# Kernel tuning notes

Measured on AMD Instinct MI355X. Metric: run time of the kernel, lower is better.

The kernel has to match this reference:

```python
import jax, jax.numpy as jnp
import numpy as np

B, D, F, FH = 8, 16, 16, 128
L = D * D
EPS = 1e-5


def _coords():
    i = np.arange(L, dtype=np.float64)
    c0 = ((i + 1) / D - D / 2) / (D / 2)
    c1 = ((i + 1) % D - D / 2) / (D / 2)
    return jnp.asarray(np.stack([c0, c1], axis=1), dtype=jnp.float32)  # (L, 2)


def setup_inputs() -> dict:
    key = jax.random.key(0)
    ks = jax.random.split(key, 16)
    s = 0.05
    fin = F + 2
    inp = {
        "x": jax.random.normal(ks[0], (B, F, D, D), jnp.float32),
        # g_fc1 weight split into the x_i half (first f+2 cols) and x_j half
        "W1a": jax.random.normal(ks[1], (fin, FH), jnp.float32) * s,
        "W1b": jax.random.normal(ks[2], (fin, FH), jnp.float32) * s,
        "b1": jnp.zeros((FH,), jnp.float32),
        "g1_gamma": jnp.ones((FH,), jnp.float32), "g1_beta": jnp.zeros((FH,), jnp.float32),
        "W2": jax.random.normal(ks[3], (FH, FH), jnp.float32) * s, "b2": jnp.zeros((FH,), jnp.float32),
        "g2_gamma": jnp.ones((FH,), jnp.float32), "g2_beta": jnp.zeros((FH,), jnp.float32),
        "W3": jax.random.normal(ks[4], (FH, FH), jnp.float32) * s, "b3": jnp.zeros((FH,), jnp.float32),
        "g3_gamma": jnp.ones((FH,), jnp.float32), "g3_beta": jnp.zeros((FH,), jnp.float32),
        "Wagg": jax.random.normal(ks[5], (L,), jnp.float32) * s, "bagg": jnp.zeros((), jnp.float32),
        "Wf": jax.random.normal(ks[6], (FH, FH), jnp.float32) * s, "bf": jnp.zeros((FH,), jnp.float32),
        "f_gamma": jnp.ones((FH,), jnp.float32), "f_beta": jnp.zeros((FH,), jnp.float32),
        "Wo2": jax.random.normal(ks[7], (FH, FH), jnp.float32) * s, "bo2": jnp.zeros((FH,), jnp.float32),
        "o2_gamma": jnp.ones((FH,), jnp.float32), "o2_beta": jnp.zeros((FH,), jnp.float32),
        "Wo3": jax.random.normal(ks[8], (FH, F), jnp.float32) * s, "bo3": jnp.zeros((F,), jnp.float32),
        "coord": _coords(),
    }
    return inp


def _bn(h, gamma, beta):
    # torch BatchNorm1d (training mode) applied over channel dim = last axis here;
    # stats over (batch, length), biased variance.
    mu = jnp.mean(h, axis=(0, 1))
    var = jnp.mean((h - mu) ** 2, axis=(0, 1))
    return gamma * (h - mu) * jax.lax.rsqrt(var + EPS) + beta


def reference(x, W1a, W1b, b1, g1_gamma, g1_beta, W2, b2, g2_gamma, g2_beta,
              W3, b3, g3_gamma, g3_beta, Wagg, bagg, Wf, bf, f_gamma, f_beta,
              Wo2, bo2, o2_gamma, o2_beta, Wo3, bo3, coord):
    b, f, d = x.shape[0], x.shape[1], x.shape[2]
    l = d * d
    x_flat = x.reshape(b, f, l).transpose(0, 2, 1)                     # (b, L, f)
    x_flat = jnp.concatenate([x_flat, jnp.broadcast_to(coord, (b, l, 2))], axis=2)  # (b, L, f+2)
    # g_fc1 on cat([x_i, x_j]): x_i varies along pair-dim2 (index l), x_j along dim1 (index k)
    hi = x_flat @ W1a                                                  # (b, L, FH)
    hj = x_flat @ W1b                                                  # (b, L, FH)
    h = hi[:, None, :, :] + hj[:, :, None, :] + b1                     # (b, L, L, FH)
    h = h.reshape(b, l * l, -1)
    h = jax.nn.relu(_bn(h, g1_gamma, g1_beta))
    h = jax.nn.relu(_bn(h @ W2 + b2, g2_gamma, g2_beta))
    h = jax.nn.relu(_bn(h @ W3 + b3, g3_gamma, g3_beta))
    x_g = h.reshape(b, l, l, -1)                                       # (b, k, l, FH)
    # affine_aggregate: Linear(L -> 1) over the l (dim2) axis after permute
    x_agg = jnp.einsum('bklf,l->bkf', x_g, Wagg) + bagg                # (b, L, FH)
    x_f = jax.nn.relu(_bn(x_agg @ Wf + bf, f_gamma, f_beta))
    xo = jax.nn.relu(_bn(x_f @ Wo2 + bo2, o2_gamma, o2_beta))
    out = xo @ Wo3 + bo3                                               # (b, L, f)
    return out.reshape(b, d, d, f).transpose(0, 3, 1, 2)               # (b, f, d, d)
```

## Files before the change

kernel.cpp:

```cpp
#include <hip/hip_runtime.h>
#include <hip/hip_bf16.h>

typedef __bf16 bf16x8 __attribute__((ext_vector_type(8)));
typedef float  f32x4  __attribute__((ext_vector_type(4)));

static constexpr size_t MB = 1u << 20;
static constexpr size_t HI_OFF  = 0;
static constexpr size_t HJ_OFF  = HI_OFF + MB;
static constexpr size_t Z_OFF   = HJ_OFF + MB;
static constexpr size_t PS_OFF  = Z_OFF + (size_t)524288 * 128 * 2;
static constexpr size_t PQ_OFF  = PS_OFF + (size_t)4096 * 128 * 4;
static constexpr size_t S1I_OFF = PQ_OFF + (size_t)4096 * 128 * 4;
static constexpr size_t S2I_OFF = S1I_OFF + 32768;
static constexpr size_t S1J_OFF = S2I_OFF + 32768;
static constexpr size_t S2J_OFF = S1J_OFF + 32768;
static constexpr size_t A1_OFF  = S2J_OFF + 32768;
static constexpr size_t D1_OFF  = A1_OFF + 512;
static constexpr size_t A2_OFF  = D1_OFF + 512;
static constexpr size_t C2_OFF  = A2_OFF + 512;
static constexpr size_t A3_OFF  = C2_OFF + 512;
static constexpr size_t C3_OFF  = A3_OFF + 512;
static constexpr size_t AF_OFF  = C3_OFF + 512;
static constexpr size_t CF_OFF  = AF_OFF + 512;
static constexpr size_t AO_OFF  = CF_OFF + 512;
static constexpr size_t CO_OFF  = AO_OFF + 512;
static constexpr size_t W2T_OFF = CO_OFF + 512;
static constexpr size_t W3T_OFF = W2T_OFF + 32768;
static constexpr size_t XAGG_OFF = W3T_OFF + 32768;
static constexpr size_t Y1_OFF  = XAGG_OFF + MB;
static constexpr size_t Y2_OFF  = Y1_OFF + MB;
static constexpr size_t TPS_OFF = Y2_OFF + MB;
static constexpr size_t TPQ_OFF = TPS_OFF + 65536;

__global__ void build_h(const float* __restrict__ x, const float* __restrict__ coord,
                        const float* __restrict__ W1a, const float* __restrict__ W1b,
                        float* __restrict__ hi, float* __restrict__ hj)
{
    __shared__ float xr[18];
    int bl = blockIdx.x;
    int b = bl >> 8, l = bl & 255;
    int t = threadIdx.x;
    if (t < 18)
        xr[t] = (t < 16) ? x[((size_t)b * 16 + t) * 256 + l] : coord[l * 2 + (t - 16)];
    __syncthreads();
    float ai = 0.f, aj = 0.f;
#pragma unroll
    for (int c = 0; c < 18; ++c) {
        float xv = xr[c];
        ai += xv * W1a[c * 128 + t];
        aj += xv * W1b[c * 128 + t];
    }
    hi[(size_t)bl * 128 + t] = ai;
    hj[(size_t)bl * 128 + t] = aj;
}

__global__ void stats1(const float* __restrict__ hi, const float* __restrict__ hj,
                       float* __restrict__ S1i, float* __restrict__ S2i,
                       float* __restrict__ S1j, float* __restrict__ S2j)
{
    int g = blockIdx.x;
    int b = g >> 3, lg = g & 7;
    int f = threadIdx.x;
    float s1i = 0, s2i = 0, s1j = 0, s2j = 0;
#pragma unroll 4
    for (int i = 0; i < 32; ++i) {
        int l = lg * 32 + i;
        float vi = hi[((size_t)b * 256 + l) * 128 + f];
        float vj = hj[((size_t)b * 256 + l) * 128 + f];
        s1i += vi; s2i += vi * vi;
        s1j += vj; s2j += vj * vj;
    }
    S1i[g * 128 + f] = s1i; S2i[g * 128 + f] = s2i;
    S1j[g * 128 + f] = s1j; S2j[g * 128 + f] = s2j;
}

__global__ void bn1_finalize(const float* __restrict__ S1i, const float* __restrict__ S2i,
                             const float* __restrict__ S1j, const float* __restrict__ S2j,
                             const float* __restrict__ g, const float* __restrict__ be,
                             float* __restrict__ a1, float* __restrict__ d1)
{
    int f = threadIdx.x;
    float s1i = 0, s2i = 0, s1j = 0, s2j = 0;
    float mib[8], mjb[8];
#pragma unroll
    for (int b = 0; b < 8; ++b) {
        float sb = 0, sbj = 0;
#pragma unroll
        for (int lg = 0; lg < 8; ++lg) {
            int gg = b * 8 + lg;
            sb  += S1i[gg * 128 + f]; s2i += S2i[gg * 128 + f];
            sbj += S1j[gg * 128 + f]; s2j += S2j[gg * 128 + f];
        }
        mib[b] = sb * (1.f / 256.f); mjb[b] = sbj * (1.f / 256.f);
        s1i += sb; s1j += sbj;
    }
    const float invN = 1.f / 2048.f;
    float mi = s1i * invN, mj = s1j * invN;
    float vu = s2i * invN - mi * mi;
    float vv = s2j * invN - mj * mj;
    float cr = 0.f;
#pragma unroll
    for (int b = 0; b < 8; ++b) cr += (mib[b] - mi) * (mjb[b] - mj);
    cr *= (1.f / 8.f);
    float var = vu + vv + 2.f * cr;
    float av = g[f] * rsqrtf(var + 1e-5f);
    a1[f] = av;
    d1[f] = be[f] - av * (mi + mj);
}

__global__ void transpose_w(const float* __restrict__ W2, const float* __restrict__ W3,
                            __bf16* __restrict__ W2t, __bf16* __restrict__ W3t)
{
    int f = blockIdx.x, k = threadIdx.x;
    W2t[f * 128 + k] = (__bf16)W2[k * 128 + f];
    W3t[f * 128 + k] = (__bf16)W3[k * 128 + f];
}

__global__ __launch_bounds__(256, 4) void pair_gemm1(
    const float* __restrict__ hi, const float* __restrict__ hj,
    const float* __restrict__ a1, const float* __restrict__ d1,
    const __bf16* __restrict__ W2t,
    __bf16* __restrict__ Z, float* __restrict__ ps, float* __restrict__ pq)
{
    __shared__ __align__(16) char hA[32768];

    int blk = blockIdx.x;
    int half = blk & 1;
    int bk = blk >> 1;
    int b = bk >> 8;
    int t = threadIdx.x;
    int lane = t & 63;
    int wave = t >> 6;
    int fc = (t & 15) * 8;
    int rg = t >> 4;
    int cl = lane & 15;
    int kg = lane >> 4;
    int colbase = wave * 32;

    bf16x8 Bf[2][4];
#pragma unroll
    for (int n = 0; n < 2; ++n) {
        const __bf16* wp = W2t + (colbase + n * 16 + cl) * 128 + kg * 8;
#pragma unroll
        for (int kk = 0; kk < 4; ++kk)
            Bf[n][kk] = *reinterpret_cast<const bf16x8*>(wp + kk * 32);
    }

    float a1v[8], qv[8];
    const float* hjrow = hj + (size_t)bk * 128 + fc;
    const float* d1p = d1 + fc;
    const float* a1p = a1 + fc;
#pragma unroll
    for (int j = 0; j < 8; ++j) { a1v[j] = a1p[j]; qv[j] = a1v[j] * hjrow[j] + d1p[j]; }

    const float* hib = hi + ((size_t)b * 256 + half * 128) * 128;
#pragma unroll
    for (int rr = 0; rr < 128; rr += 16) {
        int row = rr + rg;
        const float* src = hib + row * 128 + fc;
        bf16x8 v;
#pragma unroll
        for (int j = 0; j < 8; ++j) {
            float h = fmaxf(a1v[j] * src[j] + qv[j], 0.f);
            v[j] = (__bf16)h;
        }
        int byte = (row * 256 + fc * 2) ^ ((row & 7) << 4);
        *reinterpret_cast<bf16x8*>(hA + byte) = v;
    }
    __syncthreads();

    f32x4 acc[8][2] = {};
#pragma unroll
    for (int kk = 0; kk < 128; kk += 32) {
        bf16x8 af[8];
#pragma unroll
        for (int m = 0; m < 8; ++m) {
            int row = m * 16 + cl;
            int byte = (row * 256 + (kk + kg * 8) * 2) ^ ((row & 7) << 4);
            af[m] = *reinterpret_cast<const bf16x8*>(hA + byte);
        }
#pragma unroll
        for (int m = 0; m < 8; ++m)
#pragma unroll
            for (int n = 0; n < 2; ++n)
                acc[m][n] = __builtin_amdgcn_mfma_f32_16x16x32_bf16(af[m], Bf[n][kk >> 5], acc[m][n], 0, 0, 0);
    }

    __bf16* zb = Z + ((size_t)bk * 256 + half * 128) * 128;
    int r0 = kg * 4;
    float s[2] = {}, q[2] = {};
#pragma unroll
    for (int m = 0; m < 8; ++m)
#pragma unroll
        for (int r = 0; r < 4; ++r) {
            int row = m * 16 + r0 + r;
#pragma unroll
            for (int n = 0; n < 2; ++n) {
                float v = acc[m][n][r];
                zb[row * 128 + colbase + n * 16 + cl] = (__bf16)v;
                s[n] += v; q[n] += v * v;
            }
        }
#pragma unroll
    for (int n = 0; n < 2; ++n) {
        float sv = s[n], qv2 = q[n];
        sv += __shfl_xor(sv, 16); sv += __shfl_xor(sv, 32);
        qv2 += __shfl_xor(qv2, 16); qv2 += __shfl_xor(qv2, 32);
        if (lane < 16) {
            ps[(size_t)blk * 128 + colbase + n * 16 + cl] = sv;
            pq[(size_t)blk * 128 + colbase + n * 16 + cl] = qv2;
        }
    }
}

__global__ __launch_bounds__(256, 4) void pair_gemm2(
    __bf16* __restrict__ Z,
    const float* __restrict__ a2, const float* __restrict__ c2,
    const __bf16* __restrict__ W3t,
    float* __restrict__ ps, float* __restrict__ pq)
{
    __shared__ __align__(16) char hA[32768];

    int blk = blockIdx.x;
    int half = blk & 1;
    int bk = blk >> 1;
    int t = threadIdx.x;
    int lane = t & 63;
    int wave = t >> 6;
    int fc = (t & 15) * 8;
    int rg = t >> 4;
    int cl = lane & 15;
    int kg = lane >> 4;
    int colbase = wave * 32;

    bf16x8 Bf[2][4];
#pragma unroll
    for (int n = 0; n < 2; ++n) {
        const __bf16* wp = W3t + (colbase + n * 16 + cl) * 128 + kg * 8;
#pragma unroll
        for (int kk = 0; kk < 4; ++kk)
            Bf[n][kk] = *reinterpret_cast<const bf16x8*>(wp + kk * 32);
    }

    float a2v[8], c2v[8];
#pragma unroll
    for (int j = 0; j < 8; ++j) { a2v[j] = a2[fc + j]; c2v[j] = c2[fc + j]; }

    __bf16* zbase = Z + ((size_t)bk * 256 + half * 128) * 128;
#pragma unroll
    for (int rr = 0; rr < 128; rr += 16) {
        int row = rr + rg;
        bf16x8 zv = *reinterpret_cast<const bf16x8*>(zbase + row * 128 + fc);
        bf16x8 v;
#pragma unroll
        for (int j = 0; j < 8; ++j) {
            float h = fmaxf(a2v[j] * (float)zv[j] + c2v[j], 0.f);
            v[j] = (__bf16)h;
        }
        int byte = (row * 256 + fc * 2) ^ ((row & 7) << 4);
        *reinterpret_cast<bf16x8*>(hA + byte) = v;
    }
    __syncthreads();

    f32x4 acc[8][2] = {};
#pragma unroll
    for (int kk = 0; kk < 128; kk += 32) {
        bf16x8 af[8];
#pragma unroll
        for (int m = 0; m < 8; ++m) {
            int row = m * 16 + cl;
            int byte = (row * 256 + (kk + kg * 8) * 2) ^ ((row & 7) << 4);
            af[m] = *reinterpret_cast<const bf16x8*>(hA + byte);
        }
#pragma unroll
        for (int m = 0; m < 8; ++m)
#pragma unroll
            for (int n = 0; n < 2; ++n)
                acc[m][n] = __builtin_amdgcn_mfma_f32_16x16x32_bf16(af[m], Bf[n][kk >> 5], acc[m][n], 0, 0, 0);
    }

    int r0 = kg * 4;
    float s[2] = {}, q[2] = {};
#pragma unroll
    for (int m = 0; m < 8; ++m)
#pragma unroll
        for (int r = 0; r < 4; ++r) {
            int row = m * 16 + r0 + r;
#pragma unroll
            for (int n = 0; n < 2; ++n) {
                float v = acc[m][n][r];
                zbase[row * 128 + colbase + n * 16 + cl] = (__bf16)v;
                s[n] += v; q[n] += v * v;
            }
        }
#pragma unroll
    for (int n = 0; n < 2; ++n) {
        float sv = s[n], qv2 = q[n];
        sv += __shfl_xor(sv, 16); sv += __shfl_xor(sv, 32);
        qv2 += __shfl_xor(qv2, 16); qv2 += __shfl_xor(qv2, 32);
        if (lane < 16) {
            ps[(size_t)blk * 128 + colbase + n * 16 + cl] = sv;
            pq[(size_t)blk * 128 + colbase + n * 16 + cl] = qv2;
        }
    }
}

__global__ void finalize_bn(const float* __restrict__ ps, const float* __restrict__ pq,
                            int nblk, float inv_count,
                            const float* __restrict__ gamma, const float* __restrict__ beta,
                            float* __restrict__ a, float* __restrict__ c)
{
    __shared__ float rs[256], rq[256];
    int f = blockIdx.x, t = threadIdx.x;
    float s = 0, q = 0;
    for (int i = t; i < nblk; i += 256) {
        s += ps[(size_t)i * 128 + f];
        q += pq[(size_t)i * 128 + f];
    }
    rs[t] = s; rq[t] = q;
    __syncthreads();
    for (int st = 128; st > 0; st >>= 1) {
        if (t < st) { rs[t] += rs[t + st]; rq[t] += rq[t + st]; }
        __syncthreads();
    }
    if (t == 0) {
        float mean = rs[0] * inv_count;
        float var = rq[0] * inv_count - mean * mean;
        float av = gamma[f] * rsqrtf(var + 1e-5f);
        a[f] = av;
        c[f] = beta[f] - av * mean;
    }
}

__global__ __launch_bounds__(256) void aggregate(
    const __bf16* __restrict__ Z,
    const float* __restrict__ a3, const float* __restrict__ c3,
    const float* __restrict__ Wagg, const float* __restrict__ bagg,
    float* __restrict__ xagg)
{
    __shared__ float red[16 * 128];
    int bk = blockIdx.x;
    int t = threadIdx.x;
    int fc = t & 15;
    int g = t >> 4;
    float av[8], cv[8];
#pragma unroll
    for (int j = 0; j < 8; ++j) { av[j] = a3[fc * 8 + j]; cv[j] = c3[fc * 8 + j]; }

    const __bf16* zb = Z + (size_t)bk * 256 * 128;
    float acc[8] = {};
#pragma unroll 4
    for (int i = 0; i < 16; ++i) {
        int l = g * 16 + i;
        bf16x8 zv = *reinterpret_cast<const bf16x8*>(zb + (size_t)l * 128 + fc * 8);
        float w = Wagg[l];
#pragma unroll
        for (int j = 0; j < 8; ++j)
            acc[j] += fmaxf(av[j] * (float)zv[j] + cv[j], 0.f) * w;
    }
#pragma unroll
    for (int j = 0; j < 8; ++j) red[g * 128 + fc * 8 + j] = acc[j];
    __syncthreads();
    if (t < 128) {
        float s = 0;
#pragma unroll
        for (int gg = 0; gg < 16; ++gg) s += red[gg * 128 + t];
        xagg[(size_t)bk * 128 + t] = s + bagg[0];
    }
}

__global__ void tail_gemm(const float* __restrict__ X,
                          const float* __restrict__ aIn, const float* __restrict__ cIn, int relu_in,
                          const float* __restrict__ W, const float* __restrict__ bias,
                          float* __restrict__ Y, float* __restrict__ ps, float* __restrict__ pq)
{
    __shared__ float xs[2048];
    __shared__ float rsum[256];
    int blk = blockIdx.x, t = threadIdx.x;
    for (int i = t; i < 2048; i += 256) {
        float v = X[(size_t)blk * 2048 + i];
        if (relu_in) { int f = i & 127; v = fmaxf(aIn[f] * v + cIn[f], 0.f); }
        xs[i] = v;
    }
    __syncthreads();
    int col = t & 127, hf = t >> 7;
    float bv = bias[col];
    float acc[8];
#pragma unroll
    for (int r = 0; r < 8; ++r) acc[r] = bv;
    for (int k = 0; k < 128; ++k) {
        float w = W[k * 128 + col];
#pragma unroll
        for (int r = 0; r < 8; ++r) acc[r] += xs[(hf * 8 + r) * 128 + k] * w;
    }
    float s = 0, q = 0;
#pragma unroll
    for (int r = 0; r < 8; ++r) {
        Y[((size_t)blk * 16 + hf * 8 + r) * 128 + col] = acc[r];
        s += acc[r]; q += acc[r] * acc[r];
    }
    rsum[t] = s; __syncthreads();
    if (hf == 0) ps[(size_t)blk * 128 + col] = rsum[col] + rsum[128 + col];
    __syncthreads();
    rsum[t] = q; __syncthreads();
    if (hf == 0) pq[(size_t)blk * 128 + col] = rsum[col] + rsum[128 + col];
}

__global__ void tail_out(const float* __restrict__ Y2,
                         const float* __restrict__ ao, const float* __restrict__ co,
                         const float* __restrict__ Wo3, const float* __restrict__ bo3,
                         float* __restrict__ out)
{
    __shared__ float xs[2048];
    int blk = blockIdx.x, t = threadIdx.x;
    for (int i = t; i < 2048; i += 256) {
        int f = i & 127;
        xs[i] = fmaxf(ao[f] * Y2[(size_t)blk * 2048 + i] + co[f], 0.f);
    }
    __syncthreads();
    int col = t & 15, r = t >> 4;
    float acc = bo3[col];
    for (int k = 0; k < 128; ++k) acc += xs[r * 128 + k] * Wo3[k * 16 + col];
    int grow = blk * 16 + r;
    int b = grow >> 8, l = grow & 255;
    out[((size_t)b * 16 + col) * 256 + l] = acc;
}

extern "C" void kernel_launch(void* const* d_in, const int* in_sizes, int n_in,
                              void* d_out, int out_size, void* d_ws, size_t ws_size,
                              hipStream_t stream)
{
    const float* x     = (const float*)d_in[0];
    const float* W1a   = (const float*)d_in[1];
    const float* W1b   = (const float*)d_in[2];
    const float* g1g   = (const float*)d_in[4];
    const float* g1b   = (const float*)d_in[5];
    const float* W2    = (const float*)d_in[6];
    const float* g2g   = (const float*)d_in[8];
    const float* g2b   = (const float*)d_in[9];
    const float* W3    = (const float*)d_in[10];
    const float* g3g   = (const float*)d_in[12];
    const float* g3b   = (const float*)d_in[13];
    const float* Wagg  = (const float*)d_in[14];
    const float* bagg  = (const float*)d_in[15];
    const float* Wf    = (const float*)d_in[16];
    const float* bf_   = (const float*)d_in[17];
    const float* fg    = (const float*)d_in[18];
    const float* fb    = (const float*)d_in[19];
    const float* Wo2   = (const float*)d_in[20];
    const float* bo2   = (const float*)d_in[21];
    const float* og    = (const float*)d_in[22];
    const float* ob    = (const float*)d_in[23];
    const float* Wo3   = (const float*)d_in[24];
    const float* bo3   = (const float*)d_in[25];
    const float* coord = (const float*)d_in[26];

    char* ws = (char*)d_ws;
    float*  HI   = (float*)(ws + HI_OFF);
    float*  HJ   = (float*)(ws + HJ_OFF);
    __bf16* Z    = (__bf16*)(ws + Z_OFF);
    float*  PS   = (float*)(ws + PS_OFF);
    float*  PQ   = (float*)(ws + PQ_OFF);
    float*  S1I  = (float*)(ws + S1I_OFF);
    float*  S2I  = (float*)(ws + S2I_OFF);
    float*  S1J  = (float*)(ws + S1J_OFF);
    float*  S2J  = (float*)(ws + S2J_OFF);
    float*  A1   = (float*)(ws + A1_OFF);
    float*  D1   = (float*)(ws + D1_OFF);
    float*  A2   = (float*)(ws + A2_OFF);
    float*  C2   = (float*)(ws + C2_OFF);
    float*  A3   = (float*)(ws + A3_OFF);
    float*  C3   = (float*)(ws + C3_OFF);
    float*  AF   = (float*)(ws + AF_OFF);
    float*  CF   = (float*)(ws + CF_OFF);
    float*  AO   = (float*)(ws + AO_OFF);
    float*  CO   = (float*)(ws + CO_OFF);
    __bf16* W2T  = (__bf16*)(ws + W2T_OFF);
    __bf16* W3T  = (__bf16*)(ws + W3T_OFF);
    float*  XAGG = (float*)(ws + XAGG_OFF);
    float*  Y1   = (float*)(ws + Y1_OFF);
    float*  Y2   = (float*)(ws + Y2_OFF);
    float*  TPS  = (float*)(ws + TPS_OFF);
    float*  TPQ  = (float*)(ws + TPQ_OFF);

    build_h<<<2048, 128, 0, stream>>>(x, coord, W1a, W1b, HI, HJ);
    stats1<<<64, 128, 0, stream>>>(HI, HJ, S1I, S2I, S1J, S2J);
    bn1_finalize<<<1, 128, 0, stream>>>(S1I, S2I, S1J, S2J, g1g, g1b, A1, D1);
    transpose_w<<<128, 128, 0, stream>>>(W2, W3, W2T, W3T);

    pair_gemm1<<<4096, 256, 0, stream>>>(HI, HJ, A1, D1, W2T, Z, PS, PQ);
    finalize_bn<<<128, 256, 0, stream>>>(PS, PQ, 4096, 1.f / 524288.f, g2g, g2b, A2, C2);

    pair_gemm2<<<4096, 256, 0, stream>>>(Z, A2, C2, W3T, PS, PQ);
    finalize_bn<<<128, 256, 0, stream>>>(PS, PQ, 4096, 1.f / 524288.f, g3g, g3b, A3, C3);

    aggregate<<<2048, 256, 0, stream>>>(Z, A3, C3, Wagg, bagg, XAGG);

    tail_gemm<<<128, 256, 0, stream>>>(XAGG, A1, D1, 0, Wf, bf_, Y1, TPS, TPQ);
    finalize_bn<<<128, 256, 0, stream>>>(TPS, TPQ, 128, 1.f / 2048.f, fg, fb, AF, CF);

    tail_gemm<<<128, 256, 0, stream>>>(Y1, AF, CF, 1, Wo2, bo2, Y2, TPS, TPQ);
    finalize_bn<<<128, 256, 0, stream>>>(TPS, TPQ, 128, 1.f / 2048.f, og, ob, AO, CO);

    tail_out<<<128, 256, 0, stream>>>(Y2, AO, CO, Wo3, bo3, (float*)d_out);

    (void)in_sizes; (void)n_in; (void)out_size; (void)ws_size;
}
```

Baseline: 193.6 us.

## Fuse small prologue and epilogue kernels to cut launch count

Merges build_h and stats1 into one kernel that computes hi/hj and their BN1 partial sums together. It also folds bn1_finalize into the weight-transpose kernel (block 0 does the finalize) and fuses the Wf GEMM into the aggregate kernel, writing per-row partial stats into PS/PQ. The aim is to remove several launches and the intermediate xagg round trip. The cost is that the prologue now runs on only 64 blocks, and the Wf GEMM is spread across 2048 small blocks that each reread Wf.

```diff
diff --git a/kernel.cpp b/kernel.cpp
--- a/kernel.cpp
+++ b/kernel.cpp
@@ -26,94 +26,90 @@
 static constexpr size_t CO_OFF  = AO_OFF + 512;
 static constexpr size_t W2T_OFF = CO_OFF + 512;
 static constexpr size_t W3T_OFF = W2T_OFF + 32768;
-static constexpr size_t XAGG_OFF = W3T_OFF + 32768;
-static constexpr size_t Y1_OFF  = XAGG_OFF + MB;
+static constexpr size_t Y1_OFF  = W3T_OFF + 32768;
 static constexpr size_t Y2_OFF  = Y1_OFF + MB;
 static constexpr size_t TPS_OFF = Y2_OFF + MB;
 static constexpr size_t TPQ_OFF = TPS_OFF + 65536;
 
-__global__ void build_h(const float* __restrict__ x, const float* __restrict__ coord,
-                        const float* __restrict__ W1a, const float* __restrict__ W1b,
-                        float* __restrict__ hi, float* __restrict__ hj)
-{
-    __shared__ float xr[18];
-    int bl = blockIdx.x;
-    int b = bl >> 8, l = bl & 255;
-    int t = threadIdx.x;
-    if (t < 18)
-        xr[t] = (t < 16) ? x[((size_t)b * 16 + t) * 256 + l] : coord[l * 2 + (t - 16)];
-    __syncthreads();
-    float ai = 0.f, aj = 0.f;
-#pragma unroll
-    for (int c = 0; c < 18; ++c) {
-        float xv = xr[c];
-        ai += xv * W1a[c * 128 + t];
-        aj += xv * W1b[c * 128 + t];
-    }
-    hi[(size_t)bl * 128 + t] = ai;
-    hj[(size_t)bl * 128 + t] = aj;
-}
-
-__global__ void stats1(const float* __restrict__ hi, const float* __restrict__ hj,
-                       float* __restrict__ S1i, float* __restrict__ S2i,
-                       float* __restrict__ S1j, float* __restrict__ S2j)
-{
+__global__ void build_stats(const float* __restrict__ x, const float* __restrict__ coord,
+                            const float* __restrict__ W1a, const float* __restrict__ W1b,
+                            float* __restrict__ hi, float* __restrict__ hj,
+                            float* __restrict__ S1i, float* __restrict__ S2i,
+                            float* __restrict__ S1j, float* __restrict__ S2j)
+{
+    __shared__ float xls[16][32];
+    __shared__ float cls[32][2];
     int g = blockIdx.x;
     int b = g >> 3, lg = g & 7;
-    int f = threadIdx.x;
+    int t = threadIdx.x;
+    for (int i = t; i < 512; i += 128) {
+        int c = i >> 5, l = i & 31;
+        xls[c][l] = x[((size_t)(b * 16 + c)) * 256 + lg * 32 + l];
+    }
+    if (t < 64) cls[t >> 1][t & 1] = coord[(lg * 32 + (t >> 1)) * 2 + (t & 1)];
+    __syncthreads();
+
+    float wa[18], wb[18];
+#pragma unroll
+    for (int c = 0; c < 18; ++c) { wa[c] = W1a[c * 128 + t]; wb[c] = W1b[c * 128 + t]; }
+
     float s1i = 0, s2i = 0, s1j = 0, s2j = 0;
-#pragma unroll 4
-    for (int i = 0; i < 32; ++i) {
-        int l = lg * 32 + i;
-        float vi = hi[((size_t)b * 256 + l) * 128 + f];
-        float vj = hj[((size_t)b * 256 + l) * 128 + f];
-        s1i += vi; s2i += vi * vi;
-        s1j += vj; s2j += vj * vj;
-    }
-    S1i[g * 128 + f] = s1i; S2i[g * 128 + f] = s2i;
-    S1j[g * 128 + f] = s1j; S2j[g * 128 + f] = s2j;
-}
-
-__global__ void bn1_finalize(const float* __restrict__ S1i, const float* __restrict__ S2i,
-                             const float* __restrict__ S1j, const float* __restrict__ S2j,
-                             const float* __restrict__ g, const float* __restrict__ be,
-                             float* __restrict__ a1, float* __restrict__ d1)
-{
-    int f = threadIdx.x;
-    float s1i = 0, s2i = 0, s1j = 0, s2j = 0;
-    float mib[8], mjb[8];
-#pragma unroll
-    for (int b = 0; b < 8; ++b) {
-        float sb = 0, sbj = 0;
-#pragma unroll
-        for (int lg = 0; lg < 8; ++lg) {
-            int gg = b * 8 + lg;
-            sb  += S1i[gg * 128 + f]; s2i += S2i[gg * 128 + f];
-            sbj += S1j[gg * 128 + f]; s2j += S2j[gg * 128 + f];
-        }
-        mib[b] = sb * (1.f / 256.f); mjb[b] = sbj * (1.f / 256.f);
-        s1i += sb; s1j += sbj;
-    }
-    const float invN = 1.f / 2048.f;
-    float mi = s1i * invN, mj = s1j * invN;
-    float vu = s2i * invN - mi * mi;
-    float vv = s2j * invN - mj * mj;
-    float cr = 0.f;
-#pragma unroll
-    for (int b = 0; b < 8; ++b) cr += (mib[b] - mi) * (mjb[b] - mj);
-    cr *= (1.f / 8.f);
-    float var = vu + vv + 2.f * cr;
-    float av = g[f] * rsqrtf(var + 1e-5f);
-    a1[f] = av;
-    d1[f] = be[f] - av * (mi + mj);
-}
-
-__global__ void transpose_w(const float* __restrict__ W2, const float* __restrict__ W3,
-                            __bf16* __restrict__ W2t, __bf16* __restrict__ W3t)
+    for (int l = 0; l < 32; ++l) {
+        float ai = 0.f, aj = 0.f;
+#pragma unroll
+        for (int c = 0; c < 16; ++c) { float xv = xls[c][l]; ai += xv * wa[c]; aj += xv * wb[c]; }
+#pragma unroll
+        for (int c = 0; c < 2; ++c)  { float xv = cls[l][c]; ai += xv * wa[16 + c]; aj += xv * wb[16 + c]; }
+        size_t row = (size_t)b * 256 + lg * 32 + l;
+        hi[row * 128 + t] = ai;
+        hj[row * 128 + t] = aj;
+        s1i += ai; s2i += ai * ai;
+        s1j += aj; s2j += aj * aj;
+    }
+    S1i[g * 128 + t] = s1i; S2i[g * 128 + t] = s2i;
+    S1j[g * 128 + t] = s1j; S2j[g * 128 + t] = s2j;
+}
+
+__global__ void bn1_tw(const float* __restrict__ S1i, const float* __restrict__ S2i,
+                       const float* __restrict__ S1j, const float* __restrict__ S2j,
+                       const float* __restrict__ g, const float* __restrict__ be,
+                       float* __restrict__ a1, float* __restrict__ d1,
+                       const float* __restrict__ W2, const float* __restrict__ W3,
+                       __bf16* __restrict__ W2t, __bf16* __restrict__ W3t)
 {
     int f = blockIdx.x, k = threadIdx.x;
     W2t[f * 128 + k] = (__bf16)W2[k * 128 + f];
     W3t[f * 128 + k] = (__bf16)W3[k * 128 + f];
+
+    if (blockIdx.x == 0) {
+        int ff = threadIdx.x;
+        float s1i = 0, s2i = 0, s1j = 0, s2j = 0;
+        float mib[8], mjb[8];
+#pragma unroll
+        for (int b = 0; b < 8; ++b) {
+            float sb = 0, sbj = 0;
+#pragma unroll
+            for (int lg = 0; lg < 8; ++lg) {
+                int gg = b * 8 + lg;
+                sb  += S1i[gg * 128 + ff]; s2i += S2i[gg * 128 + ff];
+                sbj += S1j[gg * 128 + ff]; s2j += S2j[gg * 128 + ff];
+            }
+            mib[b] = sb * (1.f / 256.f); mjb[b] = sbj * (1.f / 256.f);
+            s1i += sb; s1j += sbj;
+        }
+        const float invN = 1.f / 2048.f;
+        float mi = s1i * invN, mj = s1j * invN;
+        float vu = s2i * invN - mi * mi;
+        float vv = s2j * invN - mj * mj;
+        float cr = 0.f;
+#pragma unroll
+        for (int b = 0; b < 8; ++b) cr += (mib[b] - mi) * (mjb[b] - mj);
+        cr *= (1.f / 8.f);
+        float var = vu + vv + 2.f * cr;
+        float av = g[ff] * rsqrtf(var + 1e-5f);
+        a1[ff] = av;
+        d1[ff] = be[ff] - av * (mi + mj);
+    }
 }
 
 __global__ __launch_bounds__(256, 4) void pair_gemm1(
@@ -332,13 +328,17 @@
     }
 }
 
-__global__ __launch_bounds__(256) void aggregate(
+__global__ __launch_bounds__(256) void aggregate_tail(
     const __bf16* __restrict__ Z,
     const float* __restrict__ a3, const float* __restrict__ c3,
     const float* __restrict__ Wagg, const float* __restrict__ bagg,
-    float* __restrict__ xagg)
+    const float* __restrict__ Wf, const float* __restrict__ bf_,
+    float* __restrict__ Y1, float* __restrict__ ps, float* __restrict__ pq)
 {
     __shared__ float red[16 * 128];
+    __shared__ float xs[128];
+    __shared__ float red2[256];
+
     int bk = blockIdx.x;
     int t = threadIdx.x;
     int fc = t & 15;
@@ -365,12 +365,27 @@
         float s = 0;
 #pragma unroll
         for (int gg = 0; gg < 16; ++gg) s += red[gg * 128 + t];
-        xagg[(size_t)bk * 128 + t] = s + bagg[0];
+        xs[t] = s + bagg[0];
+    }
+    __syncthreads();
+
+    int col = t & 127, hf = t >> 7;
+    float d = 0.f;
+#pragma unroll 4
+    for (int k = hf * 64; k < hf * 64 + 64; ++k)
+        d += xs[k] * Wf[k * 128 + col];
+    red2[t] = d;
+    __syncthreads();
+    if (hf == 0) {
+        float y = red2[col] + red2[128 + col] + bf_[col];
+        Y1[(size_t)bk * 128 + col] = y;
+        ps[(size_t)bk * 128 + col] = y;
+        pq[(size_t)bk * 128 + col] = y * y;
     }
 }
 
 __global__ void tail_gemm(const float* __restrict__ X,
-                          const float* __restrict__ aIn, const float* __restrict__ cIn, int relu_in,
+                          const float* __restrict__ aIn, const float* __restrict__ cIn,
                           const float* __restrict__ W, const float* __restrict__ bias,
                           float* __restrict__ Y, float* __restrict__ ps, float* __restrict__ pq)
 {
@@ -378,9 +393,8 @@
     __shared__ float rsum[256];
     int blk = blockIdx.x, t = threadIdx.x;
     for (int i = t; i < 2048; i += 256) {
-        float v = X[(size_t)blk * 2048 + i];
-        if (relu_in) { int f = i & 127; v = fmaxf(aIn[f] * v + cIn[f], 0.f); }
-        xs[i] = v;
+        int f = i & 127;
+        xs[i] = fmaxf(aIn[f] * X[(size_t)blk * 2048 + i] + cIn[f], 0.f);
     }
     __syncthreads();
     int col = t & 127, hf = t >> 7;
@@ -477,16 +491,13 @@
     float*  CO   = (float*)(ws + CO_OFF);
     __bf16* W2T  = (__bf16*)(ws + W2T_OFF);
     __bf16* W3T  = (__bf16*)(ws + W3T_OFF);
-    float*  XAGG = (float*)(ws + XAGG_OFF);
     float*  Y1   = (float*)(ws + Y1_OFF);
     float*  Y2   = (float*)(ws + Y2_OFF);
     float*  TPS  = (float*)(ws + TPS_OFF);
     float*  TPQ  = (float*)(ws + TPQ_OFF);
 
-    build_h<<<2048, 128, 0, stream>>>(x, coord, W1a, W1b, HI, HJ);
-    stats1<<<64, 128, 0, stream>>>(HI, HJ, S1I, S2I, S1J, S2J);
-    bn1_finalize<<<1, 128, 0, stream>>>(S1I, S2I, S1J, S2J, g1g, g1b, A1, D1);
-    transpose_w<<<128, 128, 0, stream>>>(W2, W3, W2T, W3T);
+    build_stats<<<64, 128, 0, stream>>>(x, coord, W1a, W1b, HI, HJ, S1I, S2I, S1J, S2J);
+    bn1_tw<<<128, 128, 0, stream>>>(S1I, S2I, S1J, S2J, g1g, g1b, A1, D1, W2, W3, W2T, W3T);
 
     pair_gemm1<<<4096, 256, 0, stream>>>(HI, HJ, A1, D1, W2T, Z, PS, PQ);
     finalize_bn<<<128, 256, 0, stream>>>(PS, PQ, 4096, 1.f / 524288.f, g2g, g2b, A2, C2);
@@ -494,12 +505,10 @@
     pair_gemm2<<<4096, 256, 0, stream>>>(Z, A2, C2, W3T, PS, PQ);
     finalize_bn<<<128, 256, 0, stream>>>(PS, PQ, 4096, 1.f / 524288.f, g3g, g3b, A3, C3);
 
-    aggregate<<<2048, 256, 0, stream>>>(Z, A3, C3, Wagg, bagg, XAGG);
-
-    tail_gemm<<<128, 256, 0, stream>>>(XAGG, A1, D1, 0, Wf, bf_, Y1, TPS, TPQ);
-    finalize_bn<<<128, 256, 0, stream>>>(TPS, TPQ, 128, 1.f / 2048.f, fg, fb, AF, CF);
-
-    tail_gemm<<<128, 256, 0, stream>>>(Y1, AF, CF, 1, Wo2, bo2, Y2, TPS, TPQ);
+    aggregate_tail<<<2048, 256, 0, stream>>>(Z, A3, C3, Wagg, bagg, Wf, bf_, Y1, PS, PQ);
+    finalize_bn<<<128, 256, 0, stream>>>(PS, PQ, 2048, 1.f / 2048.f, fg, fb, AF, CF);
+
+    tail_gemm<<<128, 256, 0, stream>>>(Y1, AF, CF, Wo2, bo2, Y2, TPS, TPQ);
     finalize_bn<<<128, 256, 0, stream>>>(TPS, TPQ, 128, 1.f / 2048.f, og, ob, AO, CO);
 
     tail_out<<<128, 256, 0, stream>>>(Y2, AO, CO, Wo3, bo3, (float*)d_out);
```

After: 189.1 us. -2.4%, faster.
